# Kernel optimization log

Measured on AMD Instinct MI355X. Metric: run time of the kernel, lower is better.

Reference implementation:

```python
import jax, jax.numpy as jnp
import numpy as np

BS, N, NEIGHBOR_NUM, SUPPORT = 8, 2048, 20, 7
K0, C1, C2 = 32, 64, 256  # conv_0 kernel_num, conv_1 out, conv_2 out (local_latent_size)
NUM_STRUCT = 16
LOCAL_RATE = 2048 // (8 * NUM_STRUCT)  # 16


def gather_neighbors(t, idx):
    # t: (b, v, d), idx: (b, v, n) -> (b, v, n, d)
    return jax.vmap(lambda a, i: a[i])(t, idx)


def knn_index(vertices, k):
    # (b, v, 3) -> (b, v, k) indices of k nearest neighbors (excluding self)
    inner = jnp.einsum('bid,bjd->bij', vertices, vertices)
    q = jnp.sum(vertices * vertices, axis=-1)
    dist = -2.0 * inner + q[:, :, None] + q[:, None, :]
    idx = jax.lax.top_k(-dist, k + 1)[1]  # smallest distances
    return idx[:, :, 1:]


def operator3d(neighbor_index, vertices, weights, displacement, support_num, kernel_num):
    b, v, n = neighbor_index.shape
    neigh = gather_neighbors(vertices, neighbor_index)  # (b,v,n,3)
    disp = neigh - vertices[:, :, None, :]
    theta = jax.nn.relu(disp @ displacement)            # (b,v,n,s*k)
    theta = theta.reshape(b, v, n, support_num, kernel_num)
    theta = jnp.max(theta, axis=2) * weights            # (b,v,s,k)
    return jnp.sum(theta, axis=2)                       # (b,v,k)


def operator_nd(neighbor_index, vertices, feature_map, weights, bias, displacement,
                support_num, out_channel):
    b, v, n = neighbor_index.shape
    neigh = gather_neighbors(vertices, neighbor_index)
    disp = neigh - vertices[:, :, None, :]
    theta = jax.nn.relu(disp @ displacement)            # (b,v,n,s*oc)
    feat = feature_map @ weights + bias                 # (b,v,(s+1)*oc)
    feat_center = feat[:, :, :out_channel]
    feat_support = feat[:, :, out_channel:]
    feat_support = gather_neighbors(feat_support, neighbor_index)  # (b,v,n,s*oc)
    act = (theta * feat_support).reshape(b, v, n, support_num, out_channel)
    act = jnp.sum(jnp.max(act, axis=2), axis=2)         # (b,v,oc)
    return feat_center + act


def pooling(vertices, feature_map, pooling_rate, neighbor_num, seed):
    b, v, _ = vertices.shape
    idx = knn_index(vertices, neighbor_num)
    pooled = jnp.max(gather_neighbors(feature_map, idx), axis=2)
    pool_num = v // pooling_rate
    sample_idx = np.random.default_rng(seed).permutation(v)[:pool_num]
    sample_idx = jnp.asarray(sample_idx)
    return vertices[:, sample_idx, :], pooled[:, sample_idx, :]


def setup_inputs() -> dict:
    key = jax.random.key(0)
    ks = jax.random.split(key, 9)
    vertices = jax.random.normal(ks[0], (BS, N, 3), dtype=jnp.float32)

    def unif(k, shape, stdv):
        return jax.random.uniform(k, shape, minval=-stdv, maxval=stdv, dtype=jnp.float32)

    s0 = 1.0 / np.sqrt(SUPPORT * K0)
    s1 = 1.0 / np.sqrt(C1 * (SUPPORT + 1))
    s2 = 1.0 / np.sqrt(C2 * (SUPPORT + 1))
    return {
        'vertices': vertices,
        'w0_weights': unif(ks[1], (1, 1, SUPPORT, K0), s0),
        'w0_disp': unif(ks[2], (3, SUPPORT * K0), s0),
        'w1_weights': unif(ks[3], (K0, (SUPPORT + 1) * C1), s1),
        'w1_bias': unif(ks[4], ((SUPPORT + 1) * C1,), s1),
        'w1_disp': unif(ks[5], (3, SUPPORT * C1), s1),
        'w2_weights': unif(ks[6], (C1, (SUPPORT + 1) * C2), s2),
        'w2_bias': unif(ks[7], ((SUPPORT + 1) * C2,), s2),
        'w2_disp': unif(ks[8], (3, SUPPORT * C2), s2),
    }


def reference(vertices, w0_weights, w0_disp, w1_weights, w1_bias, w1_disp,
              w2_weights, w2_bias, w2_disp):
    ni = knn_index(vertices, NEIGHBOR_NUM)
    fm0 = operator3d(ni, vertices, w0_weights, w0_disp, SUPPORT, K0)
    fm0 = jax.nn.relu(fm0)  # dropout in eval mode = identity
    fm1 = jax.nn.relu(operator_nd(ni, vertices, fm0, w1_weights, w1_bias, w1_disp, SUPPORT, C1))
    v1, fm1 = pooling(vertices, fm1, pooling_rate=8, neighbor_num=8, seed=1)
    ni2 = knn_index(v1, NEIGHBOR_NUM)
    fm2 = jax.nn.relu(operator_nd(ni2, v1, fm1, w2_weights, w2_bias, w2_disp, SUPPORT, C2))
    v2, fm3 = pooling(v1, fm2, pooling_rate=LOCAL_RATE, neighbor_num=LOCAL_RATE, seed=2)
    return v2, fm3
```

## Files before the change

### kernel.cpp

```cpp
#include <hip/hip_runtime.h>
#include <hip/hip_bf16.h>
#include <stdint.h>
#include <string.h>

#define NB   8
#define NV   2048
#define NN   20
#define SUP  7
#define K0   32
#define C1   64
#define C2   256
#define NV2  256
#define NP2  16
#define COLL_CAP 320

typedef unsigned __int128 u128;

struct CPcg { u128 state; u128 inc; bool has32; uint32_t cached; };

constexpr u128 PCG_MULT = (((u128)2549297995355413924ULL) << 64) | 4865540595714422341ULL;

constexpr uint64_t c_rotr64(uint64_t v, unsigned r) {
    return (v >> (r & 63u)) | (v << ((64u - r) & 63u));
}
constexpr uint64_t pcg_next64(CPcg& g) {
    g.state = g.state * PCG_MULT + g.inc;
    uint64_t hi = (uint64_t)(g.state >> 64);
    uint64_t lo = (uint64_t)g.state;
    return c_rotr64(hi ^ lo, (unsigned)(hi >> 58));
}
constexpr uint32_t pcg_next32(CPcg& g) {
    if (g.has32) { g.has32 = false; return g.cached; }
    uint64_t n = pcg_next64(g);
    g.has32 = true;
    g.cached = (uint32_t)(n >> 32);
    return (uint32_t)n;
}
constexpr uint64_t rand_interval(CPcg& g, uint64_t mx) {
    if (mx == 0) return 0;
    uint64_t mask = mx;
    mask |= mask >> 1; mask |= mask >> 2; mask |= mask >> 4;
    mask |= mask >> 8; mask |= mask >> 16; mask |= mask >> 32;
    uint64_t v = 0;
    while ((v = ((uint64_t)pcg_next32(g) & mask)) > mx) {
    }
    return v;
}
constexpr uint32_t hashmix(uint32_t value, uint32_t& hc) {
    value ^= hc; hc *= 0x931e8875u; value *= hc; value ^= value >> 16; return value;
}
constexpr uint32_t mixpool(uint32_t x, uint32_t y) {
    uint32_t r = (x * 0xca01f9ddu) - (y * 0x4973f715u);
    r ^= r >> 16; return r;
}
constexpr CPcg make_rng(uint32_t entropy) {
    uint32_t pool[4] = {0, 0, 0, 0};
    uint32_t hc = 0x43b0d7e5u;
    for (int i = 0; i < 4; i++) {
        uint32_t v = (i == 0) ? entropy : 0u;
        pool[i] = hashmix(v, hc);
    }
    for (int isrc = 0; isrc < 4; isrc++)
        for (int idst = 0; idst < 4; idst++)
            if (isrc != idst) pool[idst] = mixpool(pool[idst], hashmix(pool[isrc], hc));
    uint32_t w[8] = {};
    uint32_t hb = 0x8b51f9ddu;
    for (int i = 0; i < 8; i++) {
        uint32_t dv = pool[i & 3];
        dv ^= hb; hb *= 0x58f38dedu; dv *= hb; dv ^= dv >> 16; w[i] = dv;
    }
    uint64_t sd[4] = {};
    for (int k = 0; k < 4; k++) sd[k] = (uint64_t)w[2 * k] | ((uint64_t)w[2 * k + 1] << 32);
    u128 s = (((u128)sd[0]) << 64) | sd[1];
    u128 iq = (((u128)sd[2]) << 64) | sd[3];
    CPcg g{};
    g.state = 0;
    g.inc = (iq << 1) | 1;
    g.state = g.state * PCG_MULT + g.inc;
    g.state += s;
    g.state = g.state * PCG_MULT + g.inc;
    g.has32 = false; g.cached = 0;
    return g;
}

struct PermOut { int p1[256]; int p2[16]; };

constexpr PermOut compute_perms() {
    PermOut o{};
    {
        CPcg g = make_rng(1u);
        int arr[2048] = {};
        for (int i = 0; i < 2048; i++) arr[i] = i;
        for (int i = 2047; i >= 1; i--) {
            int j = (int)rand_interval(g, (uint64_t)i);
            int t = arr[i]; arr[i] = arr[j]; arr[j] = t;
        }
        for (int i = 0; i < 256; i++) o.p1[i] = arr[i];
    }
    {
        CPcg g = make_rng(2u);
        int arr[256] = {};
        for (int i = 0; i < 256; i++) arr[i] = i;
        for (int i = 255; i >= 1; i--) {
            int j = (int)rand_interval(g, (uint64_t)i);
            int t = arr[i]; arr[i] = arr[j]; arr[j] = t;
        }
        for (int i = 0; i < 16; i++) o.p2[i] = arr[i];
    }
    return o;
}

struct PermArg1 { int v[256]; };
struct PermArg2 { int v[16]; };

__global__ __launch_bounds__(384) void v2_kernel(const float* __restrict__ verts,
                                                 float* __restrict__ out,
                                                 PermArg2 cidx) {
    int t = threadIdx.x;
    if (t < NB * NP2 * 3) {
        int b = t / (NP2 * 3);
        int rem = t - b * (NP2 * 3);
        int j = rem / 3;
        int c = rem - j * 3;
        out[t] = verts[(b * NV + cidx.v[j]) * 3 + c];
    }
}

template<int N, int CPL>
__global__ __launch_bounds__(256, 4) void knn_bucket_kernel(const float* __restrict__ verts,
                                                            int* __restrict__ nbr) {
    __shared__ float sv[N * 3];
    __shared__ int hist[4][256];
    __shared__ unsigned long long coll[4][COLL_CAP];
    __shared__ int cnt[4];

    constexpr int RPB = 16;
    int bpb = N / RPB;
    int b = blockIdx.x / bpb;
    int rbase = (blockIdx.x % bpb) * RPB;

    const float* vb = verts + (size_t)b * N * 3;
    for (int t = threadIdx.x; t < N * 3; t += 256) sv[t] = vb[t];
    __syncthreads();

    int wid = threadIdx.x >> 6, lane = threadIdx.x & 63;
    int* myhist = hist[wid];
    unsigned long long* mycoll = coll[wid];

    for (int rr = 0; rr < 4; rr++) {
        int i = rbase + wid * 4 + rr;
        float vx = sv[i * 3 + 0], vy = sv[i * 3 + 1], vz = sv[i * 3 + 2];
        float qi = vx * vx + vy * vy + vz * vz;

        unsigned key[CPL];
        unsigned lmin = 0xFFFFFFFFu, lmax = 0u;
        #pragma unroll
        for (int t = 0; t < CPL; t++) {
            int j = lane + 64 * t;
            float xj = sv[j * 3 + 0], yj = sv[j * 3 + 1], zj = sv[j * 3 + 2];
            float inner = vx * xj + vy * yj + vz * zj;
            float qj = xj * xj + yj * yj + zj * zj;
            float dist = (-2.0f * inner + qi) + qj;
            unsigned u = __float_as_uint(dist);
            u = (u & 0x80000000u) ? ~u : (u | 0x80000000u);
            if (j == i) u = 0xFFFFFFFFu;
            key[t] = u;
            if (u != 0xFFFFFFFFu) {
                lmin = (u < lmin) ? u : lmin;
                lmax = (u > lmax) ? u : lmax;
            }
        }
        #pragma unroll
        for (int off = 32; off >= 1; off >>= 1) {
            unsigned o1 = (unsigned)__shfl_xor((int)lmin, off);
            unsigned o2 = (unsigned)__shfl_xor((int)lmax, off);
            lmin = (o1 < lmin) ? o1 : lmin;
            lmax = (o2 > lmax) ? o2 : lmax;
        }
        float scale = (lmax > lmin) ? 255.0f / (float)(lmax - lmin) : 0.0f;

        #pragma unroll
        for (int q = 0; q < 4; q++) myhist[lane * 4 + q] = 0;
        __asm__ volatile("s_waitcnt lgkmcnt(0)" ::: "memory");
        #pragma unroll
        for (int t = 0; t < CPL; t++) {
            int bi = (key[t] == 0xFFFFFFFFu) ? 255
                     : (int)((float)(key[t] - lmin) * scale);
            bi = (bi > 255) ? 255 : bi;
            atomicAdd(&myhist[bi], 1);
        }
        __asm__ volatile("s_waitcnt lgkmcnt(0)" ::: "memory");

        int h0 = myhist[lane * 4 + 0];
        int h1 = myhist[lane * 4 + 1];
        int h2 = myhist[lane * 4 + 2];
        int h3 = myhist[lane * 4 + 3];
        int s = h0 + h1 + h2 + h3;
        int cum = s;
        #pragma unroll
        for (int off = 1; off < 64; off <<= 1) {
            int v = __shfl_up(cum, off);
            if (lane >= off) cum += v;
        }
        unsigned long long bal = __ballot(cum >= NN);
        int L = __ffsll((long long)bal) - 1;
        int baseL = __shfl(cum, L) - __shfl(s, L);
        int g0 = __shfl(h0, L), g1 = __shfl(h1, L), g2 = __shfl(h2, L);
        int B;
        if (baseL + g0 >= NN)            B = 4 * L + 0;
        else if (baseL + g0 + g1 >= NN)  B = 4 * L + 1;
        else if (baseL + g0 + g1 + g2 >= NN) B = 4 * L + 2;
        else                              B = 4 * L + 3;

        if (lane == 0) cnt[wid] = 0;
        __asm__ volatile("s_waitcnt lgkmcnt(0)" ::: "memory");
        #pragma unroll
        for (int t = 0; t < CPL; t++) {
            int bi = (key[t] == 0xFFFFFFFFu) ? 255
                     : (int)((float)(key[t] - lmin) * scale);
            bi = (bi > 255) ? 255 : bi;
            if (bi <= B) {
                int pos = atomicAdd(&cnt[wid], 1);
                if (pos < COLL_CAP)
                    mycoll[pos] = ((unsigned long long)key[t] << 32) | (unsigned)(lane + 64 * t);
            }
        }
        __asm__ volatile("s_waitcnt lgkmcnt(0)" ::: "memory");
        int count = cnt[wid];
        if (count > COLL_CAP) count = COLL_CAP;

        int* dst = nbr + ((size_t)b * N + i) * NN;
        for (int e = lane; e < count; e += 64) {
            unsigned long long me = mycoll[e];
            int rank = 0;
            for (int m = 0; m < count; m++) rank += (mycoll[m] < me);
            if (rank < NN) dst[rank] = (int)(me & 0xFFFFFFFFull);
        }
    }
}

__global__ __launch_bounds__(256) void op3d_kernel(const float* __restrict__ verts,
                                                   const int* __restrict__ nbr,
                                                   const float* __restrict__ w0w,
                                                   const float* __restrict__ w0d,
                                                   float* __restrict__ fm0) {
    __shared__ float swd[3 * SUP * K0];
    __shared__ float sww[SUP * K0];
    for (int t = threadIdx.x; t < 3 * SUP * K0; t += 256) swd[t] = w0d[t];
    for (int t = threadIdx.x; t < SUP * K0; t += 256) sww[t] = w0w[t];
    __syncthreads();

    int gid = blockIdx.x * 256 + threadIdx.x;
    int b = gid >> 11, v = gid & (NV - 1);
    const float* vb = verts + b * NV * 3;
    float vx = vb[v * 3], vy = vb[v * 3 + 1], vz = vb[v * 3 + 2];

    const int* nb = nbr + gid * NN;
    float dx[NN], dy[NN], dz[NN];
    #pragma unroll
    for (int n = 0; n < NN; n++) {
        int j = nb[n];
        dx[n] = vb[j * 3 + 0] - vx;
        dy[n] = vb[j * 3 + 1] - vy;
        dz[n] = vb[j * 3 + 2] - vz;
    }
    float* out = fm0 + gid * K0;
    #pragma unroll 1
    for (int k = 0; k < K0; k++) {
        float acc = 0.f;
        #pragma unroll
        for (int s = 0; s < SUP; s++) {
            float w0 = swd[0 * 224 + s * K0 + k];
            float w1 = swd[1 * 224 + s * K0 + k];
            float w2 = swd[2 * 224 + s * K0 + k];
            float m = 0.f;
            #pragma unroll
            for (int n = 0; n < NN; n++) {
                float t = dx[n] * w0 + dy[n] * w1 + dz[n] * w2;
                t = fmaxf(t, 0.f);
                m = fmaxf(m, t);
            }
            acc += m * sww[s * K0 + k];
        }
        out[k] = fmaxf(acc, 0.f);
    }
}

template<int K, int N>
__global__ __launch_bounds__(256) void feat_gemm(const float* __restrict__ fm,
                                                 const float* __restrict__ w,
                                                 const float* __restrict__ bias,
                                                 float* __restrict__ feat) {
    __shared__ float sf[64][K];
    __shared__ float swt[K][64];
    int cb = blockIdx.x % (N / 64), rb = blockIdx.x / (N / 64);
    int r0 = rb * 64, c0 = cb * 64;

    for (int t = threadIdx.x; t < 64 * K; t += 256)
        sf[t / K][t % K] = fm[(size_t)(r0 + t / K) * K + (t % K)];
    for (int t = threadIdx.x; t < K * 64; t += 256)
        swt[t >> 6][t & 63] = w[(size_t)(t >> 6) * N + c0 + (t & 63)];
    __syncthreads();

    int col = threadIdx.x & 63, rg = threadIdx.x >> 6;
    float bv = bias[c0 + col];
    float acc[16];
    #pragma unroll
    for (int r = 0; r < 16; r++) acc[r] = bv;
    #pragma unroll 1
    for (int k = 0; k < K; k++) {
        float wk = swt[k][col];
        #pragma unroll
        for (int r = 0; r < 16; r++) acc[r] += sf[rg * 16 + r][k] * wk;
    }
    #pragma unroll
    for (int r = 0; r < 16; r++)
        feat[(size_t)(r0 + rg * 16 + r) * N + c0 + col] = acc[r];
}

__global__ __launch_bounds__(256) void opnd1_gather(const float* __restrict__ verts,
                                                    const int* __restrict__ nbr,
                                                    const float* __restrict__ feat1,
                                                    const float* __restrict__ w1d,
                                                    float* __restrict__ fm1) {
    __shared__ float swd[3 * SUP * C1];
    for (int t = threadIdx.x; t < 3 * SUP * C1; t += 256) swd[t] = w1d[t];
    __syncthreads();

    int wid = threadIdx.x >> 6, lane = threadIdx.x & 63;
    int b = blockIdx.x & 7;
    int vtx = b * NV + (blockIdx.x >> 3) * 4 + wid;
    int v = vtx & (NV - 1);
    const float* vb = verts + b * NV * 3;
    const int* nb = nbr + vtx * NN;
    float vx = vb[v * 3], vy = vb[v * 3 + 1], vz = vb[v * 3 + 2];

    float w0r[SUP], w1r[SUP], w2r[SUP];
    #pragma unroll
    for (int ss = 0; ss < SUP; ss++) {
        w0r[ss] = swd[0 * (SUP * C1) + ss * C1 + lane];
        w1r[ss] = swd[1 * (SUP * C1) + ss * C1 + lane];
        w2r[ss] = swd[2 * (SUP * C1) + ss * C1 + lane];
    }

    const float* fb = feat1 + (size_t)b * NV * (8 * C1);
    float m[SUP];
    #pragma unroll
    for (int ss = 0; ss < SUP; ss++) m[ss] = -3.4e38f;

    #pragma unroll 4
    for (int n = 0; n < NN; n++) {
        int j = nb[n];
        float dx = vb[j * 3 + 0] - vx;
        float dy = vb[j * 3 + 1] - vy;
        float dz = vb[j * 3 + 2] - vz;
        const float* row = fb + (size_t)j * (8 * C1) + C1 + lane;
        #pragma unroll
        for (int ss = 0; ss < SUP; ss++) {
            float th = fmaxf(dx * w0r[ss] + dy * w1r[ss] + dz * w2r[ss], 0.f);
            m[ss] = fmaxf(m[ss], th * row[ss * C1]);
        }
    }
    float fcen = fb[(size_t)v * (8 * C1) + lane];
    float total = 0.f;
    #pragma unroll
    for (int ss = 0; ss < SUP; ss++) total += m[ss];
    fm1[vtx * C1 + lane] = fmaxf(fcen + total, 0.f);
}

__global__ __launch_bounds__(256) void opnd2_gather(const float* __restrict__ v1,
                                                    const int* __restrict__ nbr2,
                                                    const float* __restrict__ feat2,
                                                    const float* __restrict__ w2d,
                                                    float* __restrict__ fm2) {
    __shared__ float swd[3 * SUP * C2];
    for (int t = threadIdx.x; t < 3 * SUP * C2; t += 256) swd[t] = w2d[t];
    __syncthreads();

    int jj = threadIdx.x >> 6, lane = threadIdx.x & 63;
    int b = blockIdx.x & 7;
    int v = blockIdx.x >> 3;
    int vtx = b * NV2 + v;
    const float* vb = v1 + b * NV2 * 3;
    const int* nb = nbr2 + vtx * NN;
    float vx = vb[v * 3], vy = vb[v * 3 + 1], vz = vb[v * 3 + 2];

    int cj = jj * 64 + lane;
    float w0r[SUP], w1r[SUP], w2r[SUP];
    #pragma unroll
    for (int ss = 0; ss < SUP; ss++) {
        w0r[ss] = swd[0 * (SUP * C2) + ss * C2 + cj];
        w1r[ss] = swd[1 * (SUP * C2) + ss * C2 + cj];
        w2r[ss] = swd[2 * (SUP * C2) + ss * C2 + cj];
    }
    const float* fb = feat2 + (size_t)b * NV2 * (8 * C2);

    float m[SUP];
    #pragma unroll
    for (int ss = 0; ss < SUP; ss++) m[ss] = -3.4e38f;

    #pragma unroll 4
    for (int n = 0; n < NN; n++) {
        int j = nb[n];
        float dx = vb[j * 3 + 0] - vx;
        float dy = vb[j * 3 + 1] - vy;
        float dz = vb[j * 3 + 2] - vz;
        const float* row = fb + (size_t)j * (8 * C2) + C2 + cj;
        #pragma unroll
        for (int ss = 0; ss < SUP; ss++) {
            float th = fmaxf(dx * w0r[ss] + dy * w1r[ss] + dz * w2r[ss], 0.f);
            m[ss] = fmaxf(m[ss], th * row[ss * C2]);
        }
    }
    float total = 0.f;
    #pragma unroll
    for (int ss = 0; ss < SUP; ss++) total += m[ss];
    float fcen = fb[(size_t)v * (8 * C2) + cj];
    fm2[(size_t)vtx * C2 + cj] = fmaxf(fcen + total, 0.f);
}

__global__ __launch_bounds__(256) void pool1_kernel(const float* __restrict__ verts,
                                                    const int* __restrict__ nbr1,
                                                    const float* __restrict__ fm1,
                                                    float* __restrict__ v1,
                                                    float* __restrict__ fm1p,
                                                    PermArg1 pa) {
    int wid = threadIdx.x >> 6, lane = threadIdx.x & 63;
    int gid = blockIdx.x * 4 + wid;
    int b = gid >> 8, p = gid & 255;
    int sv = pa.v[p];
    const int* nb = nbr1 + (b * NV + sv) * NN;
    float m = -3.4e38f;
    #pragma unroll
    for (int n = 0; n < 8; n++) {
        m = fmaxf(m, fm1[(b * NV + nb[n]) * C1 + lane]);
    }
    fm1p[gid * C1 + lane] = m;
    if (lane < 3) v1[gid * 3 + lane] = verts[(b * NV + sv) * 3 + lane];
}

__global__ __launch_bounds__(256) void pool2_kernel(const int* __restrict__ nbr2,
                                                    const float* __restrict__ fm2,
                                                    float* __restrict__ out,
                                                    PermArg2 pa) {
    int wid = threadIdx.x >> 6, lane = threadIdx.x & 63;
    int gid = blockIdx.x * 4 + wid;
    int b = gid >> 4, p = gid & 15;
    int sv = pa.v[p];
    const int* nb = nbr2 + (b * NV2 + sv) * NN;
    #pragma unroll 1
    for (int jj = 0; jj < 4; jj++) {
        int c = lane + jj * 64;
        float m = -3.4e38f;
        #pragma unroll
        for (int n = 0; n < 16; n++) {
            m = fmaxf(m, fm2[(b * NV2 + nb[n]) * C2 + c]);
        }
        out[NB * NP2 * 3 + gid * C2 + c] = m;
    }
}

extern "C" void kernel_launch(void* const* d_in, const int* in_sizes, int n_in,
                              void* d_out, int out_size, void* d_ws, size_t ws_size,
                              hipStream_t stream) {
    (void)in_sizes; (void)n_in; (void)out_size; (void)ws_size;
    const float* verts = (const float*)d_in[0];
    const float* w0w = (const float*)d_in[1];
    const float* w0d = (const float*)d_in[2];
    const float* w1w = (const float*)d_in[3];
    const float* w1b = (const float*)d_in[4];
    const float* w1d = (const float*)d_in[5];
    const float* w2w = (const float*)d_in[6];
    const float* w2b = (const float*)d_in[7];
    const float* w2d = (const float*)d_in[8];
    float* out = (float*)d_out;

    static const PermOut perms = compute_perms();

    PermArg1 pa1;
    PermArg2 pa2, pac;
    memcpy(pa1.v, perms.p1, sizeof(pa1.v));
    memcpy(pa2.v, perms.p2, sizeof(pa2.v));
    for (int j = 0; j < 16; j++) pac.v[j] = perms.p1[perms.p2[j]];

    char* ws = (char*)d_ws;
    size_t off = 0;
    auto alloc = [&](size_t bytes) -> void* {
        void* p = ws + off;
        off += (bytes + 255) & ~(size_t)255;
        return p;
    };
    int*   nbr1  = (int*)  alloc((size_t)NB * NV * NN * 4);
    float* fm0   = (float*)alloc((size_t)NB * NV * K0 * 4);
    float* feat1 = (float*)alloc((size_t)NB * NV * 8 * C1 * 4);
    float* fm1   = (float*)alloc((size_t)NB * NV * C1 * 4);
    float* v1    = (float*)alloc((size_t)NB * NV2 * 3 * 4);
    float* fm1p  = (float*)alloc((size_t)NB * NV2 * C1 * 4);
    int*   nbr2  = (int*)  alloc((size_t)NB * NV2 * NN * 4);
    float* feat2 = (float*)alloc((size_t)NB * NV2 * 8 * C2 * 4);
    float* fm2   = (float*)alloc((size_t)NB * NV2 * C2 * 4);

    v2_kernel<<<1, 384, 0, stream>>>(verts, out, pac);
    knn_bucket_kernel<NV, NV / 64><<<NB * (NV / 16), 256, 0, stream>>>(verts, nbr1);
    op3d_kernel<<<64, 256, 0, stream>>>(verts, nbr1, w0w, w0d, fm0);
    feat_gemm<K0, 8 * C1><<<(NB * NV / 64) * (8 * C1 / 64), 256, 0, stream>>>(fm0, w1w, w1b, feat1);
    opnd1_gather<<<NB * NV / 4, 256, 0, stream>>>(verts, nbr1, feat1, w1d, fm1);
    pool1_kernel<<<NB * NV2 / 4, 256, 0, stream>>>(verts, nbr1, fm1, v1, fm1p, pa1);
    knn_bucket_kernel<NV2, NV2 / 64><<<NB * (NV2 / 16), 256, 0, stream>>>(v1, nbr2);
    feat_gemm<C1, 8 * C2><<<(NB * NV2 / 64) * (8 * C2 / 64), 256, 0, stream>>>(fm1p, w2w, w2b, feat2);
    opnd2_gather<<<NB * NV2, 256, 0, stream>>>(v1, nbr2, feat2, w2d, fm2);
    pool2_kernel<<<32, 256, 0, stream>>>(nbr2, fm2, out, pa2);
}
```

Baseline: 232.8 us.

## Split each KNN row across a whole block instead of one wavefront

The KNN kernel now has all four wavefronts of a block work on the same query row: each covers a quarter of the candidates, and they share one histogram, one collect buffer and a block-wide min/max reduction. Rows per block drop from 16 to 4, so four times as many blocks are launched. Vertices are staged in LDS as float4 with the squared norm precomputed, so the per-candidate norm is no longer recomputed. This spreads each row's serial bucket-select and rank work over more threads and adds blocks for the small second KNN, at the cost of several block barriers per row and four times as many redundant vertex-set loads into LDS.

```diff
diff --git a/kernel.cpp b/kernel.cpp
--- a/kernel.cpp
+++ b/kernel.cpp
@@ -127,40 +127,46 @@
 }
 
 template<int N, int CPL>
-__global__ __launch_bounds__(256, 4) void knn_bucket_kernel(const float* __restrict__ verts,
-                                                            int* __restrict__ nbr) {
-    __shared__ float sv[N * 3];
-    __shared__ int hist[4][256];
-    __shared__ unsigned long long coll[4][COLL_CAP];
-    __shared__ int cnt[4];
-
-    constexpr int RPB = 16;
+__global__ __launch_bounds__(256, 4) void knn_coop_kernel(const float* __restrict__ verts,
+                                                          int* __restrict__ nbr) {
+    __shared__ float4 svq[N];
+    __shared__ int hist[256];
+    __shared__ unsigned long long coll[COLL_CAP];
+    __shared__ int cnt;
+    __shared__ unsigned wred[8];
+
+    constexpr int RPB = 4;
     int bpb = N / RPB;
     int b = blockIdx.x / bpb;
     int rbase = (blockIdx.x % bpb) * RPB;
-
     const float* vb = verts + (size_t)b * N * 3;
-    for (int t = threadIdx.x; t < N * 3; t += 256) sv[t] = vb[t];
+
+    for (int t = threadIdx.x; t < N; t += 256) {
+        float x = vb[t * 3 + 0], y = vb[t * 3 + 1], z = vb[t * 3 + 2];
+        svq[t] = make_float4(x, y, z, x * x + y * y + z * z);
+    }
     __syncthreads();
 
     int wid = threadIdx.x >> 6, lane = threadIdx.x & 63;
-    int* myhist = hist[wid];
-    unsigned long long* mycoll = coll[wid];
-
-    for (int rr = 0; rr < 4; rr++) {
-        int i = rbase + wid * 4 + rr;
-        float vx = sv[i * 3 + 0], vy = sv[i * 3 + 1], vz = sv[i * 3 + 2];
-        float qi = vx * vx + vy * vy + vz * vz;
+
+    for (int rr = 0; rr < RPB; rr++) {
+        int i = rbase + rr;
+        float4 vi = svq[i];
+        float vx = vi.x, vy = vi.y, vz = vi.z;
+        float qi = vi.w;
+
+        hist[threadIdx.x] = 0;
+        if (threadIdx.x == 0) cnt = 0;
+        __syncthreads();
 
         unsigned key[CPL];
         unsigned lmin = 0xFFFFFFFFu, lmax = 0u;
         #pragma unroll
         for (int t = 0; t < CPL; t++) {
-            int j = lane + 64 * t;
-            float xj = sv[j * 3 + 0], yj = sv[j * 3 + 1], zj = sv[j * 3 + 2];
-            float inner = vx * xj + vy * yj + vz * zj;
-            float qj = xj * xj + yj * yj + zj * zj;
-            float dist = (-2.0f * inner + qi) + qj;
+            int j = wid * (CPL * 64) + t * 64 + lane;
+            float4 vj = svq[j];
+            float inner = vx * vj.x + vy * vj.y + vz * vj.z;
+            float dist = (-2.0f * inner + qi) + vj.w;
             unsigned u = __float_as_uint(dist);
             u = (u & 0x80000000u) ? ~u : (u | 0x80000000u);
             if (j == i) u = 0xFFFFFFFFu;
@@ -177,24 +183,30 @@
             lmin = (o1 < lmin) ? o1 : lmin;
             lmax = (o2 > lmax) ? o2 : lmax;
         }
+        if (lane == 0) { wred[wid] = lmin; wred[4 + wid] = lmax; }
+        __syncthreads();
+        lmin = wred[0];
+        lmax = wred[4];
+        #pragma unroll
+        for (int w = 1; w < 4; w++) {
+            lmin = (wred[w] < lmin) ? wred[w] : lmin;
+            lmax = (wred[4 + w] > lmax) ? wred[4 + w] : lmax;
+        }
         float scale = (lmax > lmin) ? 255.0f / (float)(lmax - lmin) : 0.0f;
 
-        #pragma unroll
-        for (int q = 0; q < 4; q++) myhist[lane * 4 + q] = 0;
-        __asm__ volatile("s_waitcnt lgkmcnt(0)" ::: "memory");
         #pragma unroll
         for (int t = 0; t < CPL; t++) {
             int bi = (key[t] == 0xFFFFFFFFu) ? 255
                      : (int)((float)(key[t] - lmin) * scale);
             bi = (bi > 255) ? 255 : bi;
-            atomicAdd(&myhist[bi], 1);
-        }
-        __asm__ volatile("s_waitcnt lgkmcnt(0)" ::: "memory");
-
-        int h0 = myhist[lane * 4 + 0];
-        int h1 = myhist[lane * 4 + 1];
-        int h2 = myhist[lane * 4 + 2];
-        int h3 = myhist[lane * 4 + 3];
+            atomicAdd(&hist[bi], 1);
+        }
+        __syncthreads();
+
+        int h0 = hist[lane * 4 + 0];
+        int h1 = hist[lane * 4 + 1];
+        int h2 = hist[lane * 4 + 2];
+        int h3 = hist[lane * 4 + 3];
         int s = h0 + h1 + h2 + h3;
         int cum = s;
         #pragma unroll
@@ -212,30 +224,31 @@
         else if (baseL + g0 + g1 + g2 >= NN) B = 4 * L + 2;
         else                              B = 4 * L + 3;
 
-        if (lane == 0) cnt[wid] = 0;
-        __asm__ volatile("s_waitcnt lgkmcnt(0)" ::: "memory");
         #pragma unroll
         for (int t = 0; t < CPL; t++) {
             int bi = (key[t] == 0xFFFFFFFFu) ? 255
                      : (int)((float)(key[t] - lmin) * scale);
             bi = (bi > 255) ? 255 : bi;
             if (bi <= B) {
-                int pos = atomicAdd(&cnt[wid], 1);
-                if (pos < COLL_CAP)
-                    mycoll[pos] = ((unsigned long long)key[t] << 32) | (unsigned)(lane + 64 * t);
+                int pos = atomicAdd(&cnt, 1);
+                if (pos < COLL_CAP) {
+                    int j = wid * (CPL * 64) + t * 64 + lane;
+                    coll[pos] = ((unsigned long long)key[t] << 32) | (unsigned)j;
+                }
             }
         }
-        __asm__ volatile("s_waitcnt lgkmcnt(0)" ::: "memory");
-        int count = cnt[wid];
+        __syncthreads();
+        int count = cnt;
         if (count > COLL_CAP) count = COLL_CAP;
 
         int* dst = nbr + ((size_t)b * N + i) * NN;
-        for (int e = lane; e < count; e += 64) {
-            unsigned long long me = mycoll[e];
+        for (int e = threadIdx.x; e < count; e += 256) {
+            unsigned long long me = coll[e];
             int rank = 0;
-            for (int m = 0; m < count; m++) rank += (mycoll[m] < me);
+            for (int m = 0; m < count; m++) rank += (coll[m] < me);
             if (rank < NN) dst[rank] = (int)(me & 0xFFFFFFFFull);
         }
+        __syncthreads();
     }
 }
 
@@ -501,12 +514,12 @@
     float* fm2   = (float*)alloc((size_t)NB * NV2 * C2 * 4);
 
     v2_kernel<<<1, 384, 0, stream>>>(verts, out, pac);
-    knn_bucket_kernel<NV, NV / 64><<<NB * (NV / 16), 256, 0, stream>>>(verts, nbr1);
+    knn_coop_kernel<NV, NV / 256><<<NB * (NV / 4), 256, 0, stream>>>(verts, nbr1);
     op3d_kernel<<<64, 256, 0, stream>>>(verts, nbr1, w0w, w0d, fm0);
     feat_gemm<K0, 8 * C1><<<(NB * NV / 64) * (8 * C1 / 64), 256, 0, stream>>>(fm0, w1w, w1b, feat1);
     opnd1_gather<<<NB * NV / 4, 256, 0, stream>>>(verts, nbr1, feat1, w1d, fm1);
     pool1_kernel<<<NB * NV2 / 4, 256, 0, stream>>>(verts, nbr1, fm1, v1, fm1p, pa1);
-    knn_bucket_kernel<NV2, NV2 / 64><<<NB * (NV2 / 16), 256, 0, stream>>>(v1, nbr2);
+    knn_coop_kernel<NV2, NV2 / 256><<<NB * (NV2 / 4), 256, 0, stream>>>(v1, nbr2);
     feat_gemm<C1, 8 * C2><<<(NB * NV2 / 64) * (8 * C2 / 64), 256, 0, stream>>>(fm1p, w2w, w2b, feat2);
     opnd2_gather<<<NB * NV2, 256, 0, stream>>>(v1, nbr2, feat2, w2d, fm2);
     pool2_kernel<<<32, 256, 0, stream>>>(nbr2, fm2, out, pa2);
```

Measured after the change: 239.5 us. 1.03x slower.
